# Optimization experiments

Hardware: AMD Instinct MI355X
Metric: run time of the kernel (lower is better)

Reference implementation:

```python
import jax, jax.numpy as jnp
import numpy as np

BATCH, SEQ, D_MODEL, D_STATE = 8, 4096, 128, 128


def setup_inputs() -> dict:
    key = jax.random.key(0)
    ks = jax.random.split(key, 6)
    x = jax.random.normal(ks[0], (BATCH, SEQ, D_MODEL), jnp.float32)
    # Stable (negative) eigenvalues so A_discrete = exp(dt*Lambda) < 1 and powers don't overflow.
    Lam = -(jax.random.uniform(ks[1], (D_STATE,), jnp.float32) * 2.0 + 0.1)
    B = jax.random.normal(ks[2], (D_STATE, D_MODEL), jnp.float32) / np.sqrt(D_STATE)
    C = jax.random.normal(ks[3], (D_MODEL, D_STATE), jnp.float32) / np.sqrt(D_STATE)
    Dv = jax.random.normal(ks[4], (D_MODEL,), jnp.float32)
    log_dt = (jax.random.uniform(ks[5], (D_MODEL,), jnp.float32)
              * (np.log(0.001) - np.log(0.1)) + np.log(0.1)).astype(jnp.float32)
    return {"x": x, "Lam": Lam, "B": B, "C": C, "Dv": Dv, "log_dt": log_dt}


def _s4_forward(x, Lam, B, C, Dv, log_dt):
    # x: (batch, L, M) with transposed=False
    _, L, M = x.shape
    dt = jnp.exp(log_dt)                                    # (M,)
    rate = dt[:, None] * Lam[None, :]                       # (M, N) = log(A_discrete)
    ell = jnp.arange(L, dtype=x.dtype)                      # (L,)
    # powers[m, s, l] = A_discrete[m, s] ** l  (closed form of the sequential cumprod)
    powers = jnp.exp(rate[:, :, None] * ell[None, None, :])  # (M, N, L)
    # Original: einsum('ds,msl->dsl', B, powers) sums over m, giving B[d,s]*Psum[s,l];
    # then einsum('md,dsl->ml', C, .) contracts d and s -> kernel = C @ B @ Psum.
    Psum = powers.sum(axis=0)                               # (N, L)
    kernel = C @ (B @ Psum)                                 # (M, L)
    xt = jnp.transpose(x, (0, 2, 1))                        # (B, M, L)
    n = 2 * L  # zero-padded linear convolution via FFT
    y_fft = jnp.fft.rfft(xt, n=n) * jnp.fft.rfft(kernel, n=n)[None]
    y = jnp.fft.irfft(y_fft, n=n)[..., :L]                  # (B, M, L)
    y = y + Dv[None, :, None] * xt                          # skip connection D*u
    return jnp.transpose(y, (0, 2, 1))                      # (B, L, M)


def reference(x, Lam, B, C, Dv, log_dt):
    return _s4_forward(x, Lam, B, C, Dv, log_dt)
```

## Files before the change

### kernel.cpp

```cpp
#include <hip/hip_runtime.h>
#include <math.h>

#define BATCH 8
#define SEQ   4096
#define DM    128
#define DS    128
#define N2    4096
#define NT    256
#define NTP   256
#define NPAIR 2048
#define KFS   4100
#define PERT  4

__device__ __forceinline__ float2 cmulf(float2 a, float2 b) {
    return make_float2(a.x * b.x - a.y * b.y, a.x * b.y + a.y * b.x);
}
__device__ __forceinline__ float2 caddf(float2 a, float2 b) { return make_float2(a.x + b.x, a.y + b.y); }
__device__ __forceinline__ float2 csubf(float2 a, float2 b) { return make_float2(a.x - b.x, a.y - b.y); }
__device__ __forceinline__ float2 conjf2(float2 a) { return make_float2(a.x, -a.y); }
__device__ __forceinline__ float2 cisf(float t) { float s, c; __sincosf(t, &s, &c); return make_float2(c, s); }

__device__ __forceinline__ int dr12(int i) {
    unsigned br = __brev((unsigned)i) >> 20;
    return (int)(((br & 0x555u) << 1) | ((br >> 1) & 0x555u));
}


__global__ void prep_G(const float* __restrict__ Cm, const float* __restrict__ Bm,
                       float* __restrict__ G) {
    int gid = blockIdx.x * blockDim.x + threadIdx.x;
    int m = gid >> 7, j = gid & 127;
    float acc = 0.f;
    for (int i = 0; i < DS; ++i) acc += Cm[m * DS + i] * Bm[i * DM + j];
    G[gid] = acc;
}

__global__ void prep_psum(const float* __restrict__ Lam, const float* __restrict__ logdt,
                          float* __restrict__ Psum) {
    __shared__ float sdt[DM];
    int tid = threadIdx.x;
    if (tid < DM) sdt[tid] = __expf(logdt[tid]);
    __syncthreads();
    int s = blockIdx.x;
    int l = blockIdx.y * NTP + tid;
    float t = Lam[s] * (float)l;
    float acc = 0.f;
    for (int m = 0; m < DM; ++m) acc += __expf(sdt[m] * t);
    Psum[s * SEQ + l] = acc;
}

__global__ void prep_K(const float* __restrict__ G, const float* __restrict__ Psum,
                       float* __restrict__ K) {
    int m = blockIdx.y;
    int l = blockIdx.x * NTP + threadIdx.x;
    float acc = 0.f;
    for (int s = 0; s < DS; ++s) acc += G[m * DS + s] * Psum[s * SEQ + l];
    K[m * SEQ + l] = acc;
}


__device__ __forceinline__ void r4_fwd(float2* z, int tid, int q) {
    const float astep = -(float)M_PI / (2.0f * (float)q);
#pragma unroll
    for (int k = 0; k < PERT; ++k) {
        int idx = tid + k * NT;
        int j = idx & (q - 1);
        int base = ((idx & ~(q - 1)) << 2) | j;
        float2 a0 = z[base], a1 = z[base + q], a2 = z[base + 2 * q], a3 = z[base + 3 * q];
        float2 w1 = cisf(astep * (float)j);
        float2 w2 = cmulf(w1, w1);
        float2 w3 = cmulf(w1, w2);
        float2 t0 = caddf(a0, a2), t1 = csubf(a0, a2);
        float2 t2 = caddf(a1, a3), t3 = csubf(a1, a3);
        z[base]         = caddf(t0, t2);
        z[base + q]     = cmulf(make_float2(t1.x + t3.y, t1.y - t3.x), w1);
        z[base + 2 * q] = cmulf(csubf(t0, t2), w2);
        z[base + 3 * q] = cmulf(make_float2(t1.x - t3.y, t1.y + t3.x), w3);
    }
}

__device__ __forceinline__ void r4_inv(float2* z, int tid, int q) {
    const float astep = (float)M_PI / (2.0f * (float)q);
#pragma unroll
    for (int k = 0; k < PERT; ++k) {
        int idx = tid + k * NT;
        int j = idx & (q - 1);
        int base = ((idx & ~(q - 1)) << 2) | j;
        float2 y0 = z[base], y1 = z[base + q], y2 = z[base + 2 * q], y3 = z[base + 3 * q];
        float2 w1 = cisf(astep * (float)j);
        float2 w2 = cmulf(w1, w1);
        float2 w3 = cmulf(w1, w2);
        float2 b1 = cmulf(y1, w1), b2 = cmulf(y2, w2), b3 = cmulf(y3, w3);
        float2 t0 = caddf(y0, b2), t2 = csubf(y0, b2);
        float2 t1 = caddf(b1, b3);
        float2 t3 = make_float2(-(b1.y - b3.y), b1.x - b3.x);
        z[base]         = caddf(t0, t1);
        z[base + 2 * q] = csubf(t0, t1);
        z[base + q]     = caddf(t2, t3);
        z[base + 3 * q] = csubf(t2, t3);
    }
}

__device__ __forceinline__ void fwd_first_fused(float2* z, const float2* __restrict__ vrow, int tid) {
    const float astep = -(float)M_PI / 2048.0f;
#pragma unroll
    for (int c = 0; c < PERT; ++c) {
        int n = tid + c * NT;
        float2 a0 = vrow[n];
        float2 a1 = vrow[n + 1024];
        float2 w1 = cisf(astep * (float)n);
        float2 w2 = cmulf(w1, w1);
        float2 w3 = cmulf(w1, w2);
        z[n]        = caddf(a0, a1);
        z[n + 1024] = cmulf(make_float2(a0.x + a1.y, a0.y - a1.x), w1);
        z[n + 2048] = cmulf(csubf(a0, a1), w2);
        z[n + 3072] = cmulf(make_float2(a0.x - a1.y, a0.y + a1.x), w3);
    }
}


__global__ void __launch_bounds__(NT, 4) fft_Kf(const float* __restrict__ K,
                                                float2* __restrict__ Kf) {
    __shared__ __align__(16) float2 z[N2];
    int tid = threadIdx.x, m = blockIdx.x;
    const float2* krow = (const float2*)(K + (size_t)m * SEQ);

    fwd_first_fused(z, krow, tid);
    __syncthreads();
    r4_fwd(z, tid, 256); __syncthreads();
    r4_fwd(z, tid, 64);  __syncthreads();
    r4_fwd(z, tid, 16);  __syncthreads();
    r4_fwd(z, tid, 4);   __syncthreads();
    r4_fwd(z, tid, 1);   __syncthreads();

    float2* out = Kf + (size_t)m * KFS;
#pragma unroll
    for (int c = 0; c < 8; ++c) {
        int pp = tid + c * NT;
        if (pp == 0) {
            float2 v0 = z[0];
            out[0]    = make_float2(v0.x + v0.y, 0.f);
            out[4096] = make_float2(v0.x - v0.y, 0.f);
            float2 v2 = z[2];
            out[2048] = conjf2(v2);
        } else {
            int i  = ((pp >> 1) << 2) | (pp & 1);
            int k  = dr12(i);
            int kp = 4096 - k;
            int ip = dr12(kp);
            float2 va = z[i], vb = z[ip];
            float2 e  = cisf(-(float)M_PI * (float)k / 4096.0f);
            float2 cb = conjf2(vb);
            float2 s  = caddf(va, cb), d = csubf(va, cb);
            float2 pr = cmulf(e, d);
            out[k] = make_float2(0.5f * (s.x + pr.y), 0.5f * (s.y - pr.x));
            float2 ep = make_float2(-e.x, e.y);
            float2 ca = conjf2(va);
            float2 s2 = caddf(vb, ca), d2 = csubf(vb, ca);
            float2 p2 = cmulf(ep, d2);
            out[kp] = make_float2(0.5f * (s2.x + p2.y), 0.5f * (s2.y - p2.x));
        }
    }
}


__device__ __forceinline__ void pq_one(float2 Kk, float2 Kkp, float thk,
                                       float2 fap, float2 fbp,
                                       float2* P, float2* Q) {
    float2 e  = cisf(-thk);
    float2 fa = make_float2(0.5f * (1.f + e.y), -0.5f * e.x);
    float2 fb = make_float2(0.5f * (1.f - e.y),  0.5f * e.x);
    float2 ak = cmulf(Kk, fa), bk = cmulf(Kk, fb);
    float2 apv = cmulf(Kkp, fap), bpv = cmulf(Kkp, fbp);
    float2 g = make_float2(0.5f * (1.f + e.y), 0.5f * e.x);
    float2 h = make_float2(0.5f * (1.f - e.y), -0.5f * e.x);
    *P = caddf(cmulf(g, ak), cmulf(h, conjf2(bpv)));
    *Q = caddf(cmulf(g, bk), cmulf(h, conjf2(apv)));
}

__device__ __forceinline__ void pq_pair(float2 Kk, float2 Kkp, float thk, float thkp,
                                        float2* Pk, float2* Qk, float2* Pkp, float2* Qkp) {
    float2 e  = cisf(-thk);
    float2 ep = cisf(-thkp);
    float2 fa  = make_float2(0.5f * (1.f + e.y),  -0.5f * e.x);
    float2 fb  = make_float2(0.5f * (1.f - e.y),   0.5f * e.x);
    float2 fap = make_float2(0.5f * (1.f + ep.y), -0.5f * ep.x);
    float2 fbp = make_float2(0.5f * (1.f - ep.y),  0.5f * ep.x);
    pq_one(Kk,  Kkp, thk,  fap, fbp, Pk,  Qk);
    pq_one(Kkp, Kk,  thkp, fa,  fb,  Pkp, Qkp);
}

__global__ void prep_PQ(const float2* __restrict__ Kf, float4* __restrict__ PQ) {
    int m = blockIdx.x;
    int p = blockIdx.y * NTP + threadIdx.x;
    const float2* kf = Kf + (size_t)m * KFS;
    float4* dst = PQ + ((size_t)m * NPAIR + p) * 2;
    float2 Pk, Qk, Pkp, Qkp;
    if (p == 0) {
        float2 P0, Q0, Pd, Qd;
        pq_pair(kf[0], kf[4096], 0.f, (float)M_PI, &P0, &Q0, &Pd, &Qd);
        float th2 = (float)M_PI * 0.5f;
        float2 P2, Q2, Pd2, Qd2;
        pq_pair(kf[2048], kf[2048], th2, th2, &P2, &Q2, &Pd2, &Qd2);
        dst[0] = make_float4(P0.x, P0.y, Q0.x, Q0.y);
        dst[1] = make_float4(P2.x, P2.y, Q2.x, Q2.y);
    } else {
        int i  = ((p >> 1) << 2) | (p & 1);
        int k  = dr12(i);
        int kp = 4096 - k;
        pq_pair(kf[k], kf[kp],
                (float)M_PI * (float)k / 4096.0f,
                (float)M_PI * (float)kp / 4096.0f,
                &Pk, &Qk, &Pkp, &Qkp);
        dst[0] = make_float4(Pk.x, Pk.y, Qk.x, Qk.y);
        dst[1] = make_float4(Pkp.x, Pkp.y, Qkp.x, Qkp.y);
    }
}


__global__ void transpose_xin(const float* __restrict__ x, float* __restrict__ xt) {
    __shared__ float tile[32][33];
    int b = blockIdx.z;
    int l0 = blockIdx.x * 32, m0 = blockIdx.y * 32;
    int tx = threadIdx.x, ty = threadIdx.y;
    for (int r = 0; r < 4; ++r) {
        int l = l0 + ty + r * 8;
        tile[ty + r * 8][tx] = x[(size_t)b * SEQ * DM + (size_t)l * DM + m0 + tx];
    }
    __syncthreads();
    for (int r = 0; r < 4; ++r) {
        int m = m0 + ty + r * 8;
        xt[(size_t)b * DM * SEQ + (size_t)m * SEQ + l0 + tx] = tile[tx][ty + r * 8];
    }
}

__global__ void transpose_yout(const float* __restrict__ yt, float* __restrict__ out) {
    __shared__ float tile[32][33];
    int b = blockIdx.z;
    int l0 = blockIdx.x * 32, m0 = blockIdx.y * 32;
    int tx = threadIdx.x, ty = threadIdx.y;
    for (int r = 0; r < 4; ++r) {
        int m = m0 + ty + r * 8;
        tile[ty + r * 8][tx] = yt[(size_t)b * DM * SEQ + (size_t)m * SEQ + l0 + tx];
    }
    __syncthreads();
    for (int r = 0; r < 4; ++r) {
        int l = l0 + ty + r * 8;
        out[(size_t)b * SEQ * DM + (size_t)l * DM + m0 + tx] = tile[tx][ty + r * 8];
    }
}


__global__ void __launch_bounds__(NT, 5) conv_r2c(float* __restrict__ xt,
                                                  const float4* __restrict__ PQ,
                                                  const float* __restrict__ Dv) {
    __shared__ __align__(16) float2 z[N2];
    int tid = threadIdx.x;
    int m = blockIdx.x & (DM - 1);
    int b = blockIdx.x >> 7;
    float2* xrow = (float2*)(xt + (((size_t)b * DM + m) << 12));

    fwd_first_fused(z, xrow, tid);
    __syncthreads();
    r4_fwd(z, tid, 256); __syncthreads();
    r4_fwd(z, tid, 64);  __syncthreads();
    r4_fwd(z, tid, 16);  __syncthreads();
    r4_fwd(z, tid, 4);   __syncthreads();
    r4_fwd(z, tid, 1);   __syncthreads();

    {
        const float4* pq = PQ + (size_t)m * NPAIR * 2;
#pragma unroll
        for (int c = 0; c < 8; ++c) {
            int pp = tid + c * NT;
            float4 lo = pq[2 * pp];
            float4 hi = pq[2 * pp + 1];
            if (pp == 0) {
                float2 v0 = z[0];
                z[0] = caddf(cmulf(make_float2(lo.x, lo.y), v0),
                             cmulf(make_float2(lo.z, lo.w), conjf2(v0)));
                float2 v2 = z[2];
                z[2] = caddf(cmulf(make_float2(hi.x, hi.y), v2),
                             cmulf(make_float2(hi.z, hi.w), conjf2(v2)));
            } else {
                int i  = ((pp >> 1) << 2) | (pp & 1);
                int k  = dr12(i);
                int kp = 4096 - k;
                int ip = dr12(kp);
                float2 va = z[i], vb = z[ip];
                z[i]  = caddf(cmulf(make_float2(lo.x, lo.y), va),
                              cmulf(make_float2(lo.z, lo.w), conjf2(vb)));
                z[ip] = caddf(cmulf(make_float2(hi.x, hi.y), vb),
                              cmulf(make_float2(hi.z, hi.w), conjf2(va)));
            }
        }
    }
    __syncthreads();

    r4_inv(z, tid, 1);   __syncthreads();
    r4_inv(z, tid, 4);   __syncthreads();
    r4_inv(z, tid, 16);  __syncthreads();
    r4_inv(z, tid, 64);  __syncthreads();
    r4_inv(z, tid, 256); __syncthreads();

    {
        const float astep = (float)M_PI / 2048.0f;
        const float invN = 1.0f / 4096.0f;
        float dv = Dv[m];
#pragma unroll
        for (int c = 0; c < PERT; ++c) {
            int j = tid + c * NT;
            float2 y0 = z[j], y1 = z[j + 1024], y2 = z[j + 2048], y3 = z[j + 3072];
            float2 w1 = cisf(astep * (float)j);
            float2 w2 = cmulf(w1, w1);
            float2 w3 = cmulf(w1, w2);
            float2 b1 = cmulf(y1, w1), b2 = cmulf(y2, w2), b3 = cmulf(y3, w3);
            float2 t0 = caddf(y0, b2), t2 = csubf(y0, b2);
            float2 t1 = caddf(b1, b3);
            float2 t3 = make_float2(-(b1.y - b3.y), b1.x - b3.x);
            float2 r0 = caddf(t0, t1);
            float2 r1 = caddf(t2, t3);
            float2 x0 = xrow[j];
            float2 x1 = xrow[j + 1024];
            xrow[j]        = make_float2(r0.x * invN + dv * x0.x, r0.y * invN + dv * x0.y);
            xrow[j + 1024] = make_float2(r1.x * invN + dv * x1.x, r1.y * invN + dv * x1.y);
        }
    }
}

extern "C" void kernel_launch(void* const* d_in, const int* in_sizes, int n_in,
                              void* d_out, int out_size, void* d_ws, size_t ws_size,
                              hipStream_t stream) {
    const float* x     = (const float*)d_in[0];
    const float* Lam   = (const float*)d_in[1];
    const float* Bm    = (const float*)d_in[2];
    const float* Cm    = (const float*)d_in[3];
    const float* Dv    = (const float*)d_in[4];
    const float* logdt = (const float*)d_in[5];
    float* out = (float*)d_out;

    float*  ws   = (float*)d_ws;
    float*  xt   = ws;
    float2* Kf   = (float2*)(ws + 4194304);
    float4* PQ   = (float4*)(ws + 4194304 + 1049600);
    float*  K    = ws + 4194304 + 1049600 + 2097152;
    float*  Psum = K + 524288;
    float*  G    = Psum + 524288;

    hipLaunchKernelGGL(prep_G,         dim3(64),         dim3(NTP),    0, stream, Cm, Bm, G);
    hipLaunchKernelGGL(prep_psum,      dim3(128, 16),    dim3(NTP),    0, stream, Lam, logdt, Psum);
    hipLaunchKernelGGL(prep_K,         dim3(16, 128),    dim3(NTP),    0, stream, G, Psum, K);
    hipLaunchKernelGGL(fft_Kf,         dim3(128),        dim3(NT),     0, stream, K, (float2*)Kf);
    hipLaunchKernelGGL(prep_PQ,        dim3(128, 8),     dim3(NTP),    0, stream, (const float2*)Kf, PQ);
    hipLaunchKernelGGL(transpose_xin,  dim3(128, 4, 8),  dim3(32, 8),  0, stream, x, xt);
    hipLaunchKernelGGL(conv_r2c,       dim3(1024),       dim3(NT),     0, stream, xt, (const float4*)PQ, Dv);
    hipLaunchKernelGGL(transpose_yout, dim3(128, 4, 8),  dim3(32, 8),  0, stream, xt, out);
}
```

Baseline: 151.5 us.

## Switch to radix-16 FFT stages and fuse kernel FFT with PQ prep

Replaces the five radix-4 shared-memory FFT passes with three radix-16 passes that use register-resident 16-point DFTs and XOR-swizzled shared addressing, cutting the number of barriers and shared-memory round trips. The first stage exploits the zero-padded half of the input. The kernel FFT and the PQ coefficient kernels are fused, removing the Kf buffer and one launch. prep_psum now computes powers by repeated multiplication instead of one exp per element, and prep_K is tiled with shared memory and vectorized stores. Larger per-thread register arrays may lower occupancy, and recurrence-based twiddles and powers may accumulate rounding error.

```diff
diff --git a/kernel.cpp b/kernel.cpp
--- a/kernel.cpp
+++ b/kernel.cpp
@@ -8,9 +8,6 @@
 #define N2    4096
 #define NT    256
 #define NTP   256
-#define NPAIR 2048
-#define KFS   4100
-#define PERT  4
 
 __device__ __forceinline__ float2 cmulf(float2 a, float2 b) {
     return make_float2(a.x * b.x - a.y * b.y, a.x * b.y + a.y * b.x);
@@ -20,149 +17,230 @@
 __device__ __forceinline__ float2 conjf2(float2 a) { return make_float2(a.x, -a.y); }
 __device__ __forceinline__ float2 cisf(float t) { float s, c; __sincosf(t, &s, &c); return make_float2(c, s); }
 
-__device__ __forceinline__ int dr12(int i) {
-    unsigned br = __brev((unsigned)i) >> 20;
-    return (int)(((br & 0x555u) << 1) | ((br >> 1) & 0x555u));
+__device__ __forceinline__ int nibrev(int k) { return ((k & 15) << 8) | (k & 0xF0) | (k >> 8); }
+__device__ __forceinline__ int physi(int a) { return a ^ ((a >> 4) & 15); }
+
+__device__ __forceinline__ void dft16_fwd(const float2 x[16], float2 Xh[16]) {
+    const float2 W[10] = { {1.f,0.f},
+        {0.92387953f,-0.38268343f},{0.70710678f,-0.70710678f},{0.38268343f,-0.92387953f},
+        {0.f,-1.f},{-0.38268343f,-0.92387953f},{-0.70710678f,-0.70710678f},
+        {-0.92387953f,-0.38268343f},{-1.f,0.f},{-0.92387953f,0.38268343f} };
+    float2 y[16];
+#pragma unroll
+    for (int j = 0; j < 4; ++j) {
+        float2 a0 = x[j], a1 = x[j+4], a2 = x[j+8], a3 = x[j+12];
+        float2 t0 = caddf(a0,a2), t1 = csubf(a0,a2);
+        float2 t2 = caddf(a1,a3), t3 = csubf(a1,a3);
+        float2 b1 = make_float2(t1.x + t3.y, t1.y - t3.x);
+        float2 b3 = make_float2(t1.x - t3.y, t1.y + t3.x);
+        y[j]    = caddf(t0,t2);
+        y[j+4]  = cmulf(b1, W[j]);
+        y[j+8]  = cmulf(csubf(t0,t2), W[2*j]);
+        y[j+12] = cmulf(b3, W[3*j]);
+    }
+#pragma unroll
+    for (int g = 0; g < 4; ++g) {
+        float2 a0 = y[4*g], a1 = y[4*g+1], a2 = y[4*g+2], a3 = y[4*g+3];
+        float2 t0 = caddf(a0,a2), t1 = csubf(a0,a2);
+        float2 t2 = caddf(a1,a3), t3 = csubf(a1,a3);
+        Xh[4*g]   = caddf(t0,t2);
+        Xh[4*g+1] = make_float2(t1.x + t3.y, t1.y - t3.x);
+        Xh[4*g+2] = csubf(t0,t2);
+        Xh[4*g+3] = make_float2(t1.x - t3.y, t1.y + t3.x);
+    }
+}
+__device__ __forceinline__ void dft16_inv(const float2 x[16], float2 Xh[16]) {
+    const float2 W[10] = { {1.f,0.f},
+        {0.92387953f,0.38268343f},{0.70710678f,0.70710678f},{0.38268343f,0.92387953f},
+        {0.f,1.f},{-0.38268343f,0.92387953f},{-0.70710678f,0.70710678f},
+        {-0.92387953f,0.38268343f},{-1.f,0.f},{-0.92387953f,-0.38268343f} };
+    float2 y[16];
+#pragma unroll
+    for (int j = 0; j < 4; ++j) {
+        float2 a0 = x[j], a1 = x[j+4], a2 = x[j+8], a3 = x[j+12];
+        float2 t0 = caddf(a0,a2), t1 = csubf(a0,a2);
+        float2 t2 = caddf(a1,a3), t3 = csubf(a1,a3);
+        float2 b1 = make_float2(t1.x - t3.y, t1.y + t3.x);
+        float2 b3 = make_float2(t1.x + t3.y, t1.y - t3.x);
+        y[j]    = caddf(t0,t2);
+        y[j+4]  = cmulf(b1, W[j]);
+        y[j+8]  = cmulf(csubf(t0,t2), W[2*j]);
+        y[j+12] = cmulf(b3, W[3*j]);
+    }
+#pragma unroll
+    for (int g = 0; g < 4; ++g) {
+        float2 a0 = y[4*g], a1 = y[4*g+1], a2 = y[4*g+2], a3 = y[4*g+3];
+        float2 t0 = caddf(a0,a2), t1 = csubf(a0,a2);
+        float2 t2 = caddf(a1,a3), t3 = csubf(a1,a3);
+        Xh[4*g]   = caddf(t0,t2);
+        Xh[4*g+1] = make_float2(t1.x - t3.y, t1.y + t3.x);
+        Xh[4*g+2] = csubf(t0,t2);
+        Xh[4*g+3] = make_float2(t1.x + t3.y, t1.y - t3.x);
+    }
+}
+
+
+template<int Q>
+__device__ __forceinline__ void stage_fwd(float2* z, int t) {
+    float2 x[16], Xh[16];
+    int adr[16];
+    if (Q == 16) {
+        int j = t & 15, top = t >> 4;
+#pragma unroll
+        for (int r = 0; r < 16; ++r) adr[r] = (top << 8) + (r << 4) + (j ^ r);
+    } else {
+        int j4 = t & 15;
+#pragma unroll
+        for (int r = 0; r < 16; ++r) adr[r] = (t << 4) + (j4 ^ r);
+    }
+#pragma unroll
+    for (int r = 0; r < 16; ++r) x[r] = z[adr[r]];
+    dft16_fwd(x, Xh);
+    if (Q > 1) {
+        int j = t & (Q - 1);
+        float2 w1 = cisf(-(float)M_PI / (8.0f * (float)Q) * (float)j);
+        float2 w = make_float2(1.f, 0.f);
+#pragma unroll
+        for (int k = 0; k < 16; ++k) {
+            int sk = ((k & 3) << 2) | (k >> 2);
+            z[adr[k]] = cmulf(Xh[sk], w);
+            w = cmulf(w, w1);
+        }
+    } else {
+#pragma unroll
+        for (int k = 0; k < 16; ++k) {
+            int sk = ((k & 3) << 2) | (k >> 2);
+            z[adr[k]] = Xh[sk];
+        }
+    }
+}
+
+template<int Q>
+__device__ __forceinline__ void stage_inv(float2* z, int t) {
+    float2 x[16], Xh[16];
+    int adr[16];
+    if (Q == 16) {
+        int j = t & 15, top = t >> 4;
+#pragma unroll
+        for (int r = 0; r < 16; ++r) adr[r] = (top << 8) + (r << 4) + (j ^ r);
+    } else {
+        int j4 = t & 15;
+#pragma unroll
+        for (int r = 0; r < 16; ++r) adr[r] = (t << 4) + (j4 ^ r);
+    }
+    if (Q > 1) {
+        int j = t & (Q - 1);
+        float2 w1 = cisf((float)M_PI / (8.0f * (float)Q) * (float)j);
+        float2 w = make_float2(1.f, 0.f);
+#pragma unroll
+        for (int k = 0; k < 16; ++k) {
+            x[k] = cmulf(z[adr[k]], w);
+            w = cmulf(w, w1);
+        }
+    } else {
+#pragma unroll
+        for (int k = 0; k < 16; ++k) x[k] = z[adr[k]];
+    }
+    dft16_inv(x, Xh);
+#pragma unroll
+    for (int r = 0; r < 16; ++r) {
+        int sr = ((r & 3) << 2) | (r >> 2);
+        z[adr[r]] = Xh[sr];
+    }
+}
+
+__device__ __forceinline__ void fwd_first(float2* z, const float2* __restrict__ vrow, int t) {
+    float2 x[16], Xh[16];
+#pragma unroll
+    for (int r = 0; r < 8; ++r) x[r] = vrow[t + (r << 8)];
+#pragma unroll
+    for (int r = 8; r < 16; ++r) x[r] = make_float2(0.f, 0.f);
+    dft16_fwd(x, Xh);
+    int b0 = t ^ ((t >> 4) & 15);
+    float2 w1 = cisf(-(float)M_PI / 2048.0f * (float)t);
+    float2 w = make_float2(1.f, 0.f);
+#pragma unroll
+    for (int k = 0; k < 16; ++k) {
+        int sk = ((k & 3) << 2) | (k >> 2);
+        z[b0 + (k << 8)] = cmulf(Xh[sk], w);
+        w = cmulf(w, w1);
+    }
+}
+
+__device__ __forceinline__ void inv_last_store(const float2* z, float2* __restrict__ xrow,
+                                               int t, float dv) {
+    float2 x[16], Xh[16];
+    int b0 = t ^ ((t >> 4) & 15);
+    float2 w1 = cisf((float)M_PI / 2048.0f * (float)t);
+    float2 w = make_float2(1.f, 0.f);
+#pragma unroll
+    for (int k = 0; k < 16; ++k) {
+        x[k] = cmulf(z[b0 + (k << 8)], w);
+        w = cmulf(w, w1);
+    }
+    dft16_inv(x, Xh);
+    const float invN = 1.0f / 4096.0f;
+#pragma unroll
+    for (int r = 0; r < 8; ++r) {
+        int sr = ((r & 3) << 2) | (r >> 2);
+        float2 res = Xh[sr];
+        float2 xv = xrow[t + (r << 8)];
+        xrow[t + (r << 8)] = make_float2(res.x * invN + dv * xv.x, res.y * invN + dv * xv.y);
+    }
 }
 
 
 __global__ void prep_G(const float* __restrict__ Cm, const float* __restrict__ Bm,
-                       float* __restrict__ G) {
+                       float* __restrict__ GT) {
     int gid = blockIdx.x * blockDim.x + threadIdx.x;
     int m = gid >> 7, j = gid & 127;
     float acc = 0.f;
     for (int i = 0; i < DS; ++i) acc += Cm[m * DS + i] * Bm[i * DM + j];
-    G[gid] = acc;
-}
-
-__global__ void prep_psum(const float* __restrict__ Lam, const float* __restrict__ logdt,
-                          float* __restrict__ Psum) {
-    __shared__ float sdt[DM];
-    int tid = threadIdx.x;
-    if (tid < DM) sdt[tid] = __expf(logdt[tid]);
+    GT[j * DM + m] = acc;
+}
+
+__global__ void prep_psum2(const float* __restrict__ Lam, const float* __restrict__ logdt,
+                           float* __restrict__ Psum) {
+    __shared__ float E[DM];
+    int s = blockIdx.x >> 1, half = blockIdx.x & 1;
+    int t = threadIdx.x;
+    if (t < DM) E[t] = __expf(logdt[t]) * Lam[s];
     __syncthreads();
-    int s = blockIdx.x;
-    int l = blockIdx.y * NTP + tid;
-    float t = Lam[s] * (float)l;
-    float acc = 0.f;
-    for (int m = 0; m < DM; ++m) acc += __expf(sdt[m] * t);
-    Psum[s * SEQ + l] = acc;
-}
-
-__global__ void prep_K(const float* __restrict__ G, const float* __restrict__ Psum,
-                       float* __restrict__ K) {
-    int m = blockIdx.y;
-    int l = blockIdx.x * NTP + threadIdx.x;
-    float acc = 0.f;
-    for (int s = 0; s < DS; ++s) acc += G[m * DS + s] * Psum[s * SEQ + l];
-    K[m * SEQ + l] = acc;
-}
-
-
-__device__ __forceinline__ void r4_fwd(float2* z, int tid, int q) {
-    const float astep = -(float)M_PI / (2.0f * (float)q);
-#pragma unroll
-    for (int k = 0; k < PERT; ++k) {
-        int idx = tid + k * NT;
-        int j = idx & (q - 1);
-        int base = ((idx & ~(q - 1)) << 2) | j;
-        float2 a0 = z[base], a1 = z[base + q], a2 = z[base + 2 * q], a3 = z[base + 3 * q];
-        float2 w1 = cisf(astep * (float)j);
-        float2 w2 = cmulf(w1, w1);
-        float2 w3 = cmulf(w1, w2);
-        float2 t0 = caddf(a0, a2), t1 = csubf(a0, a2);
-        float2 t2 = caddf(a1, a3), t3 = csubf(a1, a3);
-        z[base]         = caddf(t0, t2);
-        z[base + q]     = cmulf(make_float2(t1.x + t3.y, t1.y - t3.x), w1);
-        z[base + 2 * q] = cmulf(csubf(t0, t2), w2);
-        z[base + 3 * q] = cmulf(make_float2(t1.x - t3.y, t1.y + t3.x), w3);
-    }
-}
-
-__device__ __forceinline__ void r4_inv(float2* z, int tid, int q) {
-    const float astep = (float)M_PI / (2.0f * (float)q);
-#pragma unroll
-    for (int k = 0; k < PERT; ++k) {
-        int idx = tid + k * NT;
-        int j = idx & (q - 1);
-        int base = ((idx & ~(q - 1)) << 2) | j;
-        float2 y0 = z[base], y1 = z[base + q], y2 = z[base + 2 * q], y3 = z[base + 3 * q];
-        float2 w1 = cisf(astep * (float)j);
-        float2 w2 = cmulf(w1, w1);
-        float2 w3 = cmulf(w1, w2);
-        float2 b1 = cmulf(y1, w1), b2 = cmulf(y2, w2), b3 = cmulf(y3, w3);
-        float2 t0 = caddf(y0, b2), t2 = csubf(y0, b2);
-        float2 t1 = caddf(b1, b3);
-        float2 t3 = make_float2(-(b1.y - b3.y), b1.x - b3.x);
-        z[base]         = caddf(t0, t1);
-        z[base + 2 * q] = csubf(t0, t1);
-        z[base + q]     = caddf(t2, t3);
-        z[base + 3 * q] = csubf(t2, t3);
-    }
-}
-
-__device__ __forceinline__ void fwd_first_fused(float2* z, const float2* __restrict__ vrow, int tid) {
-    const float astep = -(float)M_PI / 2048.0f;
-#pragma unroll
-    for (int c = 0; c < PERT; ++c) {
-        int n = tid + c * NT;
-        float2 a0 = vrow[n];
-        float2 a1 = vrow[n + 1024];
-        float2 w1 = cisf(astep * (float)n);
-        float2 w2 = cmulf(w1, w1);
-        float2 w3 = cmulf(w1, w2);
-        z[n]        = caddf(a0, a1);
-        z[n + 1024] = cmulf(make_float2(a0.x + a1.y, a0.y - a1.x), w1);
-        z[n + 2048] = cmulf(csubf(a0, a1), w2);
-        z[n + 3072] = cmulf(make_float2(a0.x - a1.y, a0.y + a1.x), w3);
-    }
-}
-
-
-__global__ void __launch_bounds__(NT, 4) fft_Kf(const float* __restrict__ K,
-                                                float2* __restrict__ Kf) {
-    __shared__ __align__(16) float2 z[N2];
-    int tid = threadIdx.x, m = blockIdx.x;
-    const float2* krow = (const float2*)(K + (size_t)m * SEQ);
-
-    fwd_first_fused(z, krow, tid);
+    int l0 = t + 2048 * half;
+    float acc[8] = {0.f,0.f,0.f,0.f,0.f,0.f,0.f,0.f};
+    for (int m = 0; m < DM; ++m) {
+        float e = E[m];
+        float w = __expf(e * (float)l0);
+        float r = __expf(e * 256.0f);
+#pragma unroll
+        for (int i = 0; i < 8; ++i) { acc[i] += w; w *= r; }
+    }
+#pragma unroll
+    for (int i = 0; i < 8; ++i) Psum[s * SEQ + l0 + 256 * i] = acc[i];
+}
+
+__global__ void prep_K2(const float* __restrict__ GT, const float* __restrict__ Psum,
+                        float* __restrict__ K) {
+    __shared__ float4 PT[DS][4];
+    int l0 = blockIdx.x * 16;
+    int t = threadIdx.x;
+    for (int idx = t; idx < 512; idx += NTP) {
+        int s = idx >> 2, q = idx & 3;
+        PT[s][q] = ((const float4*)(Psum + s * SEQ + l0))[q];
+    }
     __syncthreads();
-    r4_fwd(z, tid, 256); __syncthreads();
-    r4_fwd(z, tid, 64);  __syncthreads();
-    r4_fwd(z, tid, 16);  __syncthreads();
-    r4_fwd(z, tid, 4);   __syncthreads();
-    r4_fwd(z, tid, 1);   __syncthreads();
-
-    float2* out = Kf + (size_t)m * KFS;
-#pragma unroll
-    for (int c = 0; c < 8; ++c) {
-        int pp = tid + c * NT;
-        if (pp == 0) {
-            float2 v0 = z[0];
-            out[0]    = make_float2(v0.x + v0.y, 0.f);
-            out[4096] = make_float2(v0.x - v0.y, 0.f);
-            float2 v2 = z[2];
-            out[2048] = conjf2(v2);
-        } else {
-            int i  = ((pp >> 1) << 2) | (pp & 1);
-            int k  = dr12(i);
-            int kp = 4096 - k;
-            int ip = dr12(kp);
-            float2 va = z[i], vb = z[ip];
-            float2 e  = cisf(-(float)M_PI * (float)k / 4096.0f);
-            float2 cb = conjf2(vb);
-            float2 s  = caddf(va, cb), d = csubf(va, cb);
-            float2 pr = cmulf(e, d);
-            out[k] = make_float2(0.5f * (s.x + pr.y), 0.5f * (s.y - pr.x));
-            float2 ep = make_float2(-e.x, e.y);
-            float2 ca = conjf2(va);
-            float2 s2 = caddf(vb, ca), d2 = csubf(vb, ca);
-            float2 p2 = cmulf(ep, d2);
-            out[kp] = make_float2(0.5f * (s2.x + p2.y), 0.5f * (s2.y - p2.x));
-        }
-    }
-}
-
+    int m = t & 127, half = t >> 7;
+    float acc[8] = {0.f,0.f,0.f,0.f,0.f,0.f,0.f,0.f};
+    for (int s = 0; s < DS; ++s) {
+        float g = GT[s * DM + m];
+        float4 p0 = PT[s][half * 2], p1 = PT[s][half * 2 + 1];
+        acc[0] += g * p0.x; acc[1] += g * p0.y; acc[2] += g * p0.z; acc[3] += g * p0.w;
+        acc[4] += g * p1.x; acc[5] += g * p1.y; acc[6] += g * p1.z; acc[7] += g * p1.w;
+    }
+    float4* kp = (float4*)(K + (size_t)m * SEQ + l0 + half * 8);
+    kp[0] = make_float4(acc[0], acc[1], acc[2], acc[3]);
+    kp[1] = make_float4(acc[4], acc[5], acc[6], acc[7]);
+}
 
 __device__ __forceinline__ void pq_one(float2 Kk, float2 Kkp, float thk,
                                        float2 fap, float2 fbp,
@@ -177,7 +255,6 @@
     *P = caddf(cmulf(g, ak), cmulf(h, conjf2(bpv)));
     *Q = caddf(cmulf(g, bk), cmulf(h, conjf2(apv)));
 }
-
 __device__ __forceinline__ void pq_pair(float2 Kk, float2 Kkp, float thk, float thkp,
                                         float2* Pk, float2* Qk, float2* Pkp, float2* Qkp) {
     float2 e  = cisf(-thk);
@@ -190,33 +267,53 @@
     pq_one(Kkp, Kk,  thkp, fa,  fb,  Pkp, Qkp);
 }
 
-__global__ void prep_PQ(const float2* __restrict__ Kf, float4* __restrict__ PQ) {
-    int m = blockIdx.x;
-    int p = blockIdx.y * NTP + threadIdx.x;
-    const float2* kf = Kf + (size_t)m * KFS;
-    float4* dst = PQ + ((size_t)m * NPAIR + p) * 2;
-    float2 Pk, Qk, Pkp, Qkp;
-    if (p == 0) {
-        float2 P0, Q0, Pd, Qd;
-        pq_pair(kf[0], kf[4096], 0.f, (float)M_PI, &P0, &Q0, &Pd, &Qd);
-        float th2 = (float)M_PI * 0.5f;
-        float2 P2, Q2, Pd2, Qd2;
-        pq_pair(kf[2048], kf[2048], th2, th2, &P2, &Q2, &Pd2, &Qd2);
-        dst[0] = make_float4(P0.x, P0.y, Q0.x, Q0.y);
-        dst[1] = make_float4(P2.x, P2.y, Q2.x, Q2.y);
-    } else {
-        int i  = ((p >> 1) << 2) | (p & 1);
-        int k  = dr12(i);
-        int kp = 4096 - k;
-        pq_pair(kf[k], kf[kp],
-                (float)M_PI * (float)k / 4096.0f,
-                (float)M_PI * (float)kp / 4096.0f,
-                &Pk, &Qk, &Pkp, &Qkp);
-        dst[0] = make_float4(Pk.x, Pk.y, Qk.x, Qk.y);
-        dst[1] = make_float4(Pkp.x, Pkp.y, Qkp.x, Qkp.y);
-    }
-}
-
+__global__ void __launch_bounds__(NT, 4) fftK_PQ(const float* __restrict__ K,
+                                                 float4* __restrict__ PQ) {
+    __shared__ __align__(16) float2 z[N2];
+    int t = threadIdx.x, m = blockIdx.x;
+    const float2* krow = (const float2*)(K + (size_t)m * SEQ);
+
+    fwd_first(z, krow, t);  __syncthreads();
+    stage_fwd<16>(z, t);    __syncthreads();
+    stage_fwd<1>(z, t);     __syncthreads();
+
+    float4* dst = PQ + (size_t)m * 4096;
+#pragma unroll
+    for (int c = 0; c < 8; ++c) {
+        int k = t + 256 * c;
+        float2 Pk, Qk, Pkp, Qkp;
+        if (k == 0) {
+            float2 v0 = z[0];
+            float2 v2 = z[8];
+            float2 Ku0    = make_float2(v0.x + v0.y, 0.f);
+            float2 Ku4096 = make_float2(v0.x - v0.y, 0.f);
+            float2 Ku2048 = conjf2(v2);
+            float2 Pd, Qd;
+            pq_pair(Ku0, Ku4096, 0.f, (float)M_PI, &Pk, &Qk, &Pd, &Qd);
+            float th2 = 0.5f * (float)M_PI;
+            pq_pair(Ku2048, Ku2048, th2, th2, &Pkp, &Qkp, &Pd, &Qd);
+        } else {
+            int kp = 4096 - k;
+            float2 va = z[physi(nibrev(k))];
+            float2 vb = z[physi(nibrev(kp))];
+            float thk  = (float)M_PI * (float)k / 4096.0f;
+            float thkp = (float)M_PI - thk;
+            float2 e  = cisf(-thk);
+            float2 cb = conjf2(vb);
+            float2 s  = caddf(va, cb), d = csubf(va, cb);
+            float2 pr = cmulf(e, d);
+            float2 Kuk = make_float2(0.5f * (s.x + pr.y), 0.5f * (s.y - pr.x));
+            float2 ep = make_float2(-e.x, e.y);
+            float2 ca = conjf2(va);
+            float2 s2 = caddf(vb, ca), d2 = csubf(vb, ca);
+            float2 p2 = cmulf(ep, d2);
+            float2 Kukp = make_float2(0.5f * (s2.x + p2.y), 0.5f * (s2.y - p2.x));
+            pq_pair(Kuk, Kukp, thk, thkp, &Pk, &Qk, &Pkp, &Qkp);
+        }
+        dst[2 * k]     = make_float4(Pk.x, Pk.y, Qk.x, Qk.y);
+        dst[2 * k + 1] = make_float4(Pkp.x, Pkp.y, Qkp.x, Qkp.y);
+    }
+}
 
 __global__ void transpose_xin(const float* __restrict__ x, float* __restrict__ xt) {
     __shared__ float tile[32][33];
@@ -233,7 +330,6 @@
         xt[(size_t)b * DM * SEQ + (size_t)m * SEQ + l0 + tx] = tile[tx][ty + r * 8];
     }
 }
-
 __global__ void transpose_yout(const float* __restrict__ yt, float* __restrict__ out) {
     __shared__ float tile[32][33];
     int b = blockIdx.z;
@@ -250,43 +346,36 @@
     }
 }
 
-
-__global__ void __launch_bounds__(NT, 5) conv_r2c(float* __restrict__ xt,
-                                                  const float4* __restrict__ PQ,
-                                                  const float* __restrict__ Dv) {
+__global__ void __launch_bounds__(NT, 4) conv16(float* __restrict__ xt,
+                                                const float4* __restrict__ PQ,
+                                                const float* __restrict__ Dv) {
     __shared__ __align__(16) float2 z[N2];
-    int tid = threadIdx.x;
+    int t = threadIdx.x;
     int m = blockIdx.x & (DM - 1);
     int b = blockIdx.x >> 7;
     float2* xrow = (float2*)(xt + (((size_t)b * DM + m) << 12));
 
-    fwd_first_fused(z, xrow, tid);
-    __syncthreads();
-    r4_fwd(z, tid, 256); __syncthreads();
-    r4_fwd(z, tid, 64);  __syncthreads();
-    r4_fwd(z, tid, 16);  __syncthreads();
-    r4_fwd(z, tid, 4);   __syncthreads();
-    r4_fwd(z, tid, 1);   __syncthreads();
+    fwd_first(z, xrow, t);  __syncthreads();
+    stage_fwd<16>(z, t);    __syncthreads();
+    stage_fwd<1>(z, t);     __syncthreads();
 
     {
-        const float4* pq = PQ + (size_t)m * NPAIR * 2;
+        const float4* pq = PQ + (size_t)m * 4096;
 #pragma unroll
         for (int c = 0; c < 8; ++c) {
-            int pp = tid + c * NT;
-            float4 lo = pq[2 * pp];
-            float4 hi = pq[2 * pp + 1];
-            if (pp == 0) {
+            int k = t + 256 * c;
+            float4 lo = pq[2 * k];
+            float4 hi = pq[2 * k + 1];
+            if (k == 0) {
                 float2 v0 = z[0];
                 z[0] = caddf(cmulf(make_float2(lo.x, lo.y), v0),
                              cmulf(make_float2(lo.z, lo.w), conjf2(v0)));
-                float2 v2 = z[2];
-                z[2] = caddf(cmulf(make_float2(hi.x, hi.y), v2),
+                float2 v2 = z[8];
+                z[8] = caddf(cmulf(make_float2(hi.x, hi.y), v2),
                              cmulf(make_float2(hi.z, hi.w), conjf2(v2)));
             } else {
-                int i  = ((pp >> 1) << 2) | (pp & 1);
-                int k  = dr12(i);
-                int kp = 4096 - k;
-                int ip = dr12(kp);
+                int i  = physi(nibrev(k));
+                int ip = physi(nibrev(4096 - k));
                 float2 va = z[i], vb = z[ip];
                 z[i]  = caddf(cmulf(make_float2(lo.x, lo.y), va),
                               cmulf(make_float2(lo.z, lo.w), conjf2(vb)));
@@ -297,35 +386,9 @@
     }
     __syncthreads();
 
-    r4_inv(z, tid, 1);   __syncthreads();
-    r4_inv(z, tid, 4);   __syncthreads();
-    r4_inv(z, tid, 16);  __syncthreads();
-    r4_inv(z, tid, 64);  __syncthreads();
-    r4_inv(z, tid, 256); __syncthreads();
-
-    {
-        const float astep = (float)M_PI / 2048.0f;
-        const float invN = 1.0f / 4096.0f;
-        float dv = Dv[m];
-#pragma unroll
-        for (int c = 0; c < PERT; ++c) {
-            int j = tid + c * NT;
-            float2 y0 = z[j], y1 = z[j + 1024], y2 = z[j + 2048], y3 = z[j + 3072];
-            float2 w1 = cisf(astep * (float)j);
-            float2 w2 = cmulf(w1, w1);
-            float2 w3 = cmulf(w1, w2);
-            float2 b1 = cmulf(y1, w1), b2 = cmulf(y2, w2), b3 = cmulf(y3, w3);
-            float2 t0 = caddf(y0, b2), t2 = csubf(y0, b2);
-            float2 t1 = caddf(b1, b3);
-            float2 t3 = make_float2(-(b1.y - b3.y), b1.x - b3.x);
-            float2 r0 = caddf(t0, t1);
-            float2 r1 = caddf(t2, t3);
-            float2 x0 = xrow[j];
-            float2 x1 = xrow[j + 1024];
-            xrow[j]        = make_float2(r0.x * invN + dv * x0.x, r0.y * invN + dv * x0.y);
-            xrow[j + 1024] = make_float2(r1.x * invN + dv * x1.x, r1.y * invN + dv * x1.y);
-        }
-    }
+    stage_inv<1>(z, t);     __syncthreads();
+    stage_inv<16>(z, t);    __syncthreads();
+    inv_last_store(z, xrow, t, Dv[m]);
 }
 
 extern "C" void kernel_launch(void* const* d_in, const int* in_sizes, int n_in,
@@ -341,18 +404,16 @@
 
     float*  ws   = (float*)d_ws;
     float*  xt   = ws;
-    float2* Kf   = (float2*)(ws + 4194304);
-    float4* PQ   = (float4*)(ws + 4194304 + 1049600);
-    float*  K    = ws + 4194304 + 1049600 + 2097152;
+    float4* PQ   = (float4*)(ws + 4194304);
+    float*  K    = ws + 4194304 + 2097152;
     float*  Psum = K + 524288;
-    float*  G    = Psum + 524288;
-
-    hipLaunchKernelGGL(prep_G,         dim3(64),         dim3(NTP),    0, stream, Cm, Bm, G);
-    hipLaunchKernelGGL(prep_psum,      dim3(128, 16),    dim3(NTP),    0, stream, Lam, logdt, Psum);
-    hipLaunchKernelGGL(prep_K,         dim3(16, 128),    dim3(NTP),    0, stream, G, Psum, K);
-    hipLaunchKernelGGL(fft_Kf,         dim3(128),        dim3(NT),     0, stream, K, (float2*)Kf);
-    hipLaunchKernelGGL(prep_PQ,        dim3(128, 8),     dim3(NTP),    0, stream, (const float2*)Kf, PQ);
+    float*  GT   = Psum + 524288;
+
+    hipLaunchKernelGGL(prep_G,         dim3(64),         dim3(NTP),    0, stream, Cm, Bm, GT);
+    hipLaunchKernelGGL(prep_psum2,     dim3(256),        dim3(NTP),    0, stream, Lam, logdt, Psum);
+    hipLaunchKernelGGL(prep_K2,        dim3(256),        dim3(NTP),    0, stream, GT, Psum, K);
+    hipLaunchKernelGGL(fftK_PQ,        dim3(128),        dim3(NT),     0, stream, K, PQ);
     hipLaunchKernelGGL(transpose_xin,  dim3(128, 4, 8),  dim3(32, 8),  0, stream, x, xt);
-    hipLaunchKernelGGL(conv_r2c,       dim3(1024),       dim3(NT),     0, stream, xt, (const float4*)PQ, Dv);
+    hipLaunchKernelGGL(conv16,         dim3(1024),       dim3(NT),     0, stream, xt, PQ, Dv);
     hipLaunchKernelGGL(transpose_yout, dim3(128, 4, 8),  dim3(32, 8),  0, stream, xt, out);
 }
```

Result: faster. 141.3 us (-6.7%).
